# Performance work log

Measured on AMD Instinct MI355X. Metric: run time of the kernel, lower is better.

Reference implementation:

```python
import jax, jax.numpy as jnp
import numpy as np

N_NODES = 100000
N_EDGES = 1600000
EDGE_OUT = 48
HID = 128
NODE_OUT = 64


def setup_inputs() -> dict:
    key = jax.random.key(0)
    ks = jax.random.split(key, 8)
    x = jax.random.normal(ks[0], (N_NODES, 16), dtype=jnp.float32)
    edge_index = jax.random.randint(ks[1], (2, N_EDGES), 0, N_NODES, dtype=jnp.int64)
    edge_attr = jax.random.normal(ks[2], (N_EDGES, EDGE_OUT), dtype=jnp.float32)
    u = jax.random.normal(ks[3], (1, 8), dtype=jnp.float32)
    batch = jnp.zeros((N_NODES,), dtype=jnp.int64)
    # MLP params: Linear(3*edge_out, hid) -> ReLU -> Linear(hid, node_out)
    s1 = 1.0 / np.sqrt(3 * EDGE_OUT)
    s2 = 1.0 / np.sqrt(HID)
    W1 = jax.random.uniform(ks[4], (3 * EDGE_OUT, HID), jnp.float32, -s1, s1)
    b1 = jax.random.uniform(ks[5], (HID,), jnp.float32, -s1, s1)
    W2 = jax.random.uniform(ks[6], (HID, NODE_OUT), jnp.float32, -s2, s2)
    b2 = jax.random.uniform(ks[7], (NODE_OUT,), jnp.float32, -s2, s2)
    return {"x": x, "edge_index": edge_index, "edge_attr": edge_attr, "u": u,
            "batch": batch, "W1": W1, "b1": b1, "W2": W2, "b2": b2}


def reference(x, edge_index, edge_attr, u, batch, W1, b1, W2, b2):
    n = x.shape[0]
    col = edge_index[1]
    # fused-style aggregations over destination node indices
    out1 = jax.ops.segment_sum(edge_attr, col, num_segments=n)                      # scatter_add
    out2 = jax.ops.segment_max(edge_attr, col, num_segments=n)                      # scatter_max
    out2 = jnp.where(jnp.isneginf(out2), jnp.zeros((), edge_attr.dtype), out2)       # empty segments -> 0 (torch_scatter)
    cnt = jax.ops.segment_sum(jnp.ones((edge_attr.shape[0], 1), edge_attr.dtype), col, num_segments=n)
    out3 = out1 / jnp.maximum(cnt, jnp.ones((), edge_attr.dtype))                    # scatter_mean
    feat = jnp.concatenate([out1, out2, out3], axis=1)                               # [n, 3*edge_out]
    h = jax.nn.relu(feat @ W1 + b1)
    return h @ W2 + b2
```

## Files before the change

### kernel.cpp

```cpp
#include <hip/hip_runtime.h>
#include <math.h>

#define N_NODES 100000
#define N_EDGES 1600000
#define EO 48
constexpr int FEAT = 3 * EO;
constexpr int K1   = 160;
constexpr int HID  = 128;
constexpr int NOUT = 64;
constexpr int MAXD = 64;
constexpr int FEAT_ROWS_ALLOC = 100048;

typedef __attribute__((ext_vector_type(8))) short short8;
typedef __attribute__((ext_vector_type(4))) float floatx4;

__device__ __forceinline__ unsigned short f2h(float f) {
  _Float16 h = (_Float16)f;
  return __builtin_bit_cast(unsigned short, h);
}

__global__ void init_prep_kernel(int* __restrict__ cursor, int4* __restrict__ slots4,
                                 const float* __restrict__ W1, const float* __restrict__ W2,
                                 unsigned short* __restrict__ W1T, unsigned short* __restrict__ W2T) {
  int i = blockIdx.x * blockDim.x + threadIdx.x;
  if (i < N_NODES) cursor[i] = 0;
  if (i < N_NODES * MAXD / 4) slots4[i] = make_int4(0, 0, 0, 0);
  if (i < HID * K1) {
    int c = i / K1, k = i - c * K1;
    W1T[i] = (k < FEAT) ? f2h(W1[k * HID + c]) : (unsigned short)0;
  } else {
    int j = i - HID * K1;
    if (j < NOUT * HID) {
      int c = j / HID, k = j - c * HID;
      W2T[j] = f2h(W2[k * NOUT + c]);
    }
  }
}

__global__ void scatter_slots_kernel(const int4* __restrict__ col4, int* __restrict__ cursor,
                                     int* __restrict__ slots) {
  int i = blockIdx.x * blockDim.x + threadIdx.x;
  if (i < N_EDGES / 4) {
    int4 c = col4[i];
    int e = i * 4;
    int p;
    p = atomicAdd(&cursor[c.x], 1); if (p < MAXD) slots[c.x * MAXD + p] = e;
    p = atomicAdd(&cursor[c.y], 1); if (p < MAXD) slots[c.y * MAXD + p] = e + 1;
    p = atomicAdd(&cursor[c.z], 1); if (p < MAXD) slots[c.z * MAXD + p] = e + 2;
    p = atomicAdd(&cursor[c.w], 1); if (p < MAXD) slots[c.w * MAXD + p] = e + 3;
  }
}

__launch_bounds__(256)
__global__ void gather_kernel(const float* __restrict__ ea,
                              const int* __restrict__ slots,
                              const int* __restrict__ cursor,
                              unsigned short* __restrict__ feath) {
  const int wid  = threadIdx.x >> 6;
  const int lane = threadIdx.x & 63;
  const int g = blockIdx.x * 4 + wid;
  if (g >= N_NODES) return;

  const int eidv = slots[g * MAXD + lane];
  int deg = cursor[g];
  if (deg > MAXD) deg = MAXD;

  float s = 0.0f, m = -INFINITY;
  for (int t = 0; t < deg; t += 16) {
    float v[16];
#pragma unroll
    for (int j = 0; j < 16; ++j) {
      int e = __builtin_amdgcn_readlane(eidv, t + j);
      v[j] = (lane < EO) ? ea[(size_t)e * EO + lane] : 0.0f;
    }
#pragma unroll
    for (int j = 0; j < 16; ++j) {
      if (t + j < deg) { s += v[j]; m = fmaxf(m, v[j]); }
    }
  }

  if (lane < EO) {
    if (deg == 0) m = 0.0f;
    float mean = s / (float)(deg > 0 ? deg : 1);
    unsigned short* row = feath + (size_t)g * FEAT;
    row[lane]          = f2h(s);
    row[EO + lane]     = f2h(m);
    row[2 * EO + lane] = f2h(mean);
  }
}

__launch_bounds__(256)
__global__ void mlp_kernel(const unsigned short* __restrict__ feath,
                           const unsigned short* __restrict__ W1T,
                           const unsigned short* __restrict__ W2T,
                           const float* __restrict__ b1,
                           const float* __restrict__ b2,
                           float* __restrict__ out) {
  __shared__ unsigned short h_lds[64][HID + 8];

  const int tid  = threadIdx.x;
  const int w    = tid >> 6;
  const int lane = tid & 63;
  const int llo  = lane & 15;
  const int lhi  = lane >> 4;

  const int g0   = blockIdx.x * 64;
  int rowA = g0 + w * 16 + llo;

  floatx4 acc[8];
#pragma unroll
  for (int c = 0; c < 8; ++c) acc[c] = (floatx4)0.0f;

  const unsigned short* arow = feath + (size_t)rowA * FEAT;
#pragma unroll
  for (int ks = 0; ks < 5; ++ks) {
    short8 afrag = *(const short8*)(arow + ks * 32 + lhi * 8);
#pragma unroll
    for (int c = 0; c < 8; ++c) {
      short8 bfrag = *(const short8*)(W1T + (size_t)(c * 16 + llo) * K1 + ks * 32 + lhi * 8);
      acc[c] = __builtin_amdgcn_mfma_f32_16x16x32_f16(afrag, bfrag, acc[c], 0, 0, 0);
    }
  }

#pragma unroll
  for (int c = 0; c < 8; ++c) {
    int colc = c * 16 + llo;
    float bias = b1[colc];
#pragma unroll
    for (int r = 0; r < 4; ++r) {
      int row = w * 16 + lhi * 4 + r;
      h_lds[row][colc] = f2h(fmaxf(acc[c][r] + bias, 0.0f));
    }
  }
  __syncthreads();

  floatx4 acc2[4];
#pragma unroll
  for (int c = 0; c < 4; ++c) acc2[c] = (floatx4)0.0f;

#pragma unroll
  for (int ks = 0; ks < 4; ++ks) {
    short8 afrag = *(const short8*)&h_lds[w * 16 + llo][ks * 32 + lhi * 8];
#pragma unroll
    for (int c = 0; c < 4; ++c) {
      short8 bfrag = *(const short8*)(W2T + (size_t)(c * 16 + llo) * HID + ks * 32 + lhi * 8);
      acc2[c] = __builtin_amdgcn_mfma_f32_16x16x32_f16(afrag, bfrag, acc2[c], 0, 0, 0);
    }
  }

#pragma unroll
  for (int c = 0; c < 4; ++c) {
    int colc = c * 16 + llo;
    float bias = b2[colc];
#pragma unroll
    for (int r = 0; r < 4; ++r) {
      int g = g0 + w * 16 + lhi * 4 + r;
      if (g < N_NODES) out[(size_t)g * NOUT + colc] = acc2[c][r] + bias;
    }
  }
}

extern "C" void kernel_launch(void* const* d_in, const int* in_sizes, int n_in,
                              void* d_out, int out_size, void* d_ws, size_t ws_size,
                              hipStream_t stream) {
  const int*   eidx = (const int*)d_in[1];
  const float* ea   = (const float*)d_in[2];
  const float* W1   = (const float*)d_in[5];
  const float* b1   = (const float*)d_in[6];
  const float* W2   = (const float*)d_in[7];
  const float* b2   = (const float*)d_in[8];
  const int* col = eidx + N_EDGES;
  float* out = (float*)d_out;

  char* p = (char*)d_ws;
  int* cursor = (int*)p;  p += (size_t)N_NODES * 4;
  int* slots  = (int*)p;  p += (size_t)N_NODES * MAXD * 4;
  unsigned short* feath = (unsigned short*)p;  p += (size_t)FEAT_ROWS_ALLOC * FEAT * 2;
  unsigned short* W1T = (unsigned short*)p;    p += (size_t)HID * K1 * 2;
  unsigned short* W2T = (unsigned short*)p;

  init_prep_kernel<<<(N_NODES * MAXD / 4 + 255) / 256, 256, 0, stream>>>(
      cursor, (int4*)slots, W1, W2, W1T, W2T);
  scatter_slots_kernel<<<(N_EDGES / 4 + 255) / 256, 256, 0, stream>>>(
      (const int4*)col, cursor, slots);
  gather_kernel<<<(N_NODES + 3) / 4, 256, 0, stream>>>(ea, slots, cursor, feath);
  mlp_kernel<<<(N_NODES + 63) / 64, 256, 0, stream>>>(feath, W1T, W2T, b1, b2, out);
}
```

Before: 247.4 us.

## Scatter fp16 edge payloads into per-node buckets instead of edge-id slots

Instead of scattering edge indices into per-node slot lists and later gathering the 48-float edge rows at random, the scatter kernel now converts each edge row to fp16 and writes it straight into a per-node bucket of up to 32 rows. The gather kernel then reads each node's bucket contiguously. Edges past the bucket capacity go to a global overflow list that is scanned linearly for high-degree nodes. This removes zeroing the large slot array and the random 192-byte reads in the gather. The costs are scattered writes of 96 bytes per edge, fp16 rounding of inputs before summation, and a slow overflow path, with silent drops beyond the overflow capacity.

```diff
diff --git a/kernel.cpp b/kernel.cpp
--- a/kernel.cpp
+++ b/kernel.cpp
@@ -8,7 +8,9 @@
 constexpr int K1   = 160;
 constexpr int HID  = 128;
 constexpr int NOUT = 64;
-constexpr int MAXD = 64;
+constexpr int MAXP = 32;
+constexpr int RSTR = 48;
+constexpr int OVF_CAP = 8192;
 constexpr int FEAT_ROWS_ALLOC = 100048;
 
 typedef __attribute__((ext_vector_type(8))) short short8;
@@ -18,13 +20,19 @@
   _Float16 h = (_Float16)f;
   return __builtin_bit_cast(unsigned short, h);
 }
-
-__global__ void init_prep_kernel(int* __restrict__ cursor, int4* __restrict__ slots4,
+__device__ __forceinline__ float h2f(unsigned short u) {
+  return (float)__builtin_bit_cast(_Float16, u);
+}
+__device__ __forceinline__ unsigned int pk2(float a, float b) {
+  return (unsigned int)f2h(a) | ((unsigned int)f2h(b) << 16);
+}
+
+__global__ void init_prep_kernel(int* __restrict__ cursor, int* __restrict__ ovf_cnt,
                                  const float* __restrict__ W1, const float* __restrict__ W2,
                                  unsigned short* __restrict__ W1T, unsigned short* __restrict__ W2T) {
   int i = blockIdx.x * blockDim.x + threadIdx.x;
   if (i < N_NODES) cursor[i] = 0;
-  if (i < N_NODES * MAXD / 4) slots4[i] = make_int4(0, 0, 0, 0);
+  if (i == 0) *ovf_cnt = 0;
   if (i < HID * K1) {
     int c = i / K1, k = i - c * K1;
     W1T[i] = (k < FEAT) ? f2h(W1[k * HID + c]) : (unsigned short)0;
@@ -37,55 +45,101 @@
   }
 }
 
-__global__ void scatter_slots_kernel(const int4* __restrict__ col4, int* __restrict__ cursor,
-                                     int* __restrict__ slots) {
-  int i = blockIdx.x * blockDim.x + threadIdx.x;
-  if (i < N_EDGES / 4) {
-    int4 c = col4[i];
-    int e = i * 4;
-    int p;
-    p = atomicAdd(&cursor[c.x], 1); if (p < MAXD) slots[c.x * MAXD + p] = e;
-    p = atomicAdd(&cursor[c.y], 1); if (p < MAXD) slots[c.y * MAXD + p] = e + 1;
-    p = atomicAdd(&cursor[c.z], 1); if (p < MAXD) slots[c.z * MAXD + p] = e + 2;
-    p = atomicAdd(&cursor[c.w], 1); if (p < MAXD) slots[c.w * MAXD + p] = e + 3;
-  }
-}
-
 __launch_bounds__(256)
-__global__ void gather_kernel(const float* __restrict__ ea,
-                              const int* __restrict__ slots,
+__global__ void scatter_payload_kernel(const float* __restrict__ ea, const int* __restrict__ col,
+                                       int* __restrict__ cursor, unsigned short* __restrict__ pay,
+                                       int* __restrict__ ovf_cnt, int2* __restrict__ ovf) {
+  const int t = blockIdx.x * 256 + threadIdx.x;
+  const int e = t >> 1;
+  const int h = t & 1;
+  if (e >= N_EDGES) return;
+  const int lane = threadIdx.x & 63;
+
+  int prow = 0;
+  if (h == 0) {
+    int d = col[e];
+    int p = atomicAdd(&cursor[d], 1);
+    if (p < MAXP) {
+      prow = d * MAXP + p;
+    } else {
+      prow = -1;
+      int op = atomicAdd(ovf_cnt, 1);
+      if (op < OVF_CAP) ovf[op] = make_int2(e, d);
+    }
+  }
+  prow = __shfl(prow, lane & ~1);
+  if (prow < 0) return;
+
+  const float4* src = (const float4*)(ea + (size_t)e * EO + h * 24);
+  uint4 o0, o1, o2;
+  {
+    float4 a = src[0], b = src[1];
+    o0 = make_uint4(pk2(a.x, a.y), pk2(a.z, a.w), pk2(b.x, b.y), pk2(b.z, b.w));
+    a = src[2]; b = src[3];
+    o1 = make_uint4(pk2(a.x, a.y), pk2(a.z, a.w), pk2(b.x, b.y), pk2(b.z, b.w));
+    a = src[4]; b = src[5];
+    o2 = make_uint4(pk2(a.x, a.y), pk2(a.z, a.w), pk2(b.x, b.y), pk2(b.z, b.w));
+  }
+  uint4* dst = (uint4*)(pay + (size_t)prow * RSTR + h * 24);
+  dst[0] = o0; dst[1] = o1; dst[2] = o2;
+}
+
+__launch_bounds__(256)
+__global__ void gather_kernel(const unsigned short* __restrict__ pay,
                               const int* __restrict__ cursor,
+                              const int* __restrict__ ovf_cnt, const int2* __restrict__ ovf,
+                              const float* __restrict__ ea,
                               unsigned short* __restrict__ feath) {
   const int wid  = threadIdx.x >> 6;
   const int lane = threadIdx.x & 63;
   const int g = blockIdx.x * 4 + wid;
   if (g >= N_NODES) return;
 
-  const int eidv = slots[g * MAXD + lane];
-  int deg = cursor[g];
-  if (deg > MAXD) deg = MAXD;
-
-  float s = 0.0f, m = -INFINITY;
-  for (int t = 0; t < deg; t += 16) {
-    float v[16];
-#pragma unroll
-    for (int j = 0; j < 16; ++j) {
-      int e = __builtin_amdgcn_readlane(eidv, t + j);
-      v[j] = (lane < EO) ? ea[(size_t)e * EO + lane] : 0.0f;
-    }
-#pragma unroll
-    for (int j = 0; j < 16; ++j) {
-      if (t + j < deg) { s += v[j]; m = fmaxf(m, v[j]); }
-    }
-  }
-
-  if (lane < EO) {
-    if (deg == 0) m = 0.0f;
-    float mean = s / (float)(deg > 0 ? deg : 1);
-    unsigned short* row = feath + (size_t)g * FEAT;
-    row[lane]          = f2h(s);
-    row[EO + lane]     = f2h(m);
-    row[2 * EO + lane] = f2h(mean);
+  const int half = lane >> 5;
+  const int cl   = lane & 31;
+
+  const int deg  = cursor[g];
+  const int degc = deg < MAXP ? deg : MAXP;
+
+  float s0 = 0.0f, s1 = 0.0f, m0 = -INFINITY, m1 = -INFINITY;
+
+  const unsigned int* base = (const unsigned int*)pay + (size_t)g * MAXP * (RSTR / 2);
+  for (int tr = 0; tr < degc; tr += 2) {
+    int r = tr + half;
+    unsigned int u = base[r * (RSTR / 2) + cl];
+    if (r < degc && cl < 24) {
+      float v0 = h2f((unsigned short)(u & 0xFFFF));
+      float v1 = h2f((unsigned short)(u >> 16));
+      s0 += v0; s1 += v1;
+      m0 = fmaxf(m0, v0); m1 = fmaxf(m1, v1);
+    }
+  }
+
+  if (deg > MAXP) {
+    int k = *ovf_cnt;
+    if (k > OVF_CAP) k = OVF_CAP;
+    for (int i = 0; i < k; ++i) {
+      int2 od = ovf[i];
+      if (od.y == g && (i & 1) == half && cl < 24) {
+        float2 v = ((const float2*)(ea + (size_t)od.x * EO))[cl];
+        s0 += v.x; s1 += v.y;
+        m0 = fmaxf(m0, v.x); m1 = fmaxf(m1, v.y);
+      }
+    }
+  }
+
+  s0 += __shfl_xor(s0, 32, 64);
+  s1 += __shfl_xor(s1, 32, 64);
+  m0 = fmaxf(m0, __shfl_xor(m0, 32, 64));
+  m1 = fmaxf(m1, __shfl_xor(m1, 32, 64));
+
+  if (half == 0 && cl < 24) {
+    if (deg == 0) { m0 = 0.0f; m1 = 0.0f; }
+    float inv = 1.0f / (float)(deg > 0 ? deg : 1);
+    unsigned int* row = (unsigned int*)(feath + (size_t)g * FEAT);
+    row[cl]      = pk2(s0, s1);
+    row[24 + cl] = pk2(m0, m1);
+    row[48 + cl] = pk2(s0 * inv, s1 * inv);
   }
 }
 
@@ -173,16 +227,20 @@
   float* out = (float*)d_out;
 
   char* p = (char*)d_ws;
-  int* cursor = (int*)p;  p += (size_t)N_NODES * 4;
-  int* slots  = (int*)p;  p += (size_t)N_NODES * MAXD * 4;
+  unsigned short* pay = (unsigned short*)p;
+  p += ((size_t)N_NODES * MAXP + 2) * RSTR * 2;
   unsigned short* feath = (unsigned short*)p;  p += (size_t)FEAT_ROWS_ALLOC * FEAT * 2;
-  unsigned short* W1T = (unsigned short*)p;    p += (size_t)HID * K1 * 2;
-  unsigned short* W2T = (unsigned short*)p;
-
-  init_prep_kernel<<<(N_NODES * MAXD / 4 + 255) / 256, 256, 0, stream>>>(
-      cursor, (int4*)slots, W1, W2, W1T, W2T);
-  scatter_slots_kernel<<<(N_EDGES / 4 + 255) / 256, 256, 0, stream>>>(
-      (const int4*)col, cursor, slots);
-  gather_kernel<<<(N_NODES + 3) / 4, 256, 0, stream>>>(ea, slots, cursor, feath);
+  unsigned short* W1T   = (unsigned short*)p;  p += (size_t)HID * K1 * 2;
+  unsigned short* W2T   = (unsigned short*)p;  p += (size_t)NOUT * HID * 2;
+  int* cursor  = (int*)p;  p += (size_t)N_NODES * 4;
+  int* ovf_cnt = (int*)p;  p += 16;
+  int2* ovf    = (int2*)p;
+
+  init_prep_kernel<<<(N_NODES + 255) / 256, 256, 0, stream>>>(
+      cursor, ovf_cnt, W1, W2, W1T, W2T);
+  scatter_payload_kernel<<<(N_EDGES * 2 + 255) / 256, 256, 0, stream>>>(
+      ea, col, cursor, pay, ovf_cnt, ovf);
+  gather_kernel<<<(N_NODES + 3) / 4, 256, 0, stream>>>(
+      pay, cursor, ovf_cnt, ovf, ea, feath);
   mlp_kernel<<<(N_NODES + 63) / 64, 256, 0, stream>>>(feath, W1T, W2T, b1, b2, out);
 }
```

New measurement: 262.9 us. 1.06x slower.
